# Optimization experiments

Measured on AMD Instinct MI355X. Metric: run time of the kernel, lower is better.

Reference implementation:

```python
import jax, jax.numpy as jnp
import numpy as np
from jax import lax

VOCAB, EMBED_DIM, NUM_TAGS = 50000, 300, 16
BATCH, SEQ = 64, 512


def setup_inputs() -> dict:
    key = jax.random.key(0)
    k0, k1, k2, k3, k4 = jax.random.split(key, 5)
    text = jax.random.randint(k0, (BATCH, SEQ), 0, VOCAB)
    tags = jax.random.randint(k1, (BATCH, SEQ), 0, NUM_TAGS)
    embed_table = jax.random.normal(k2, (VOCAB, EMBED_DIM), jnp.float32) * 0.02
    W = jax.random.normal(k3, (EMBED_DIM, NUM_TAGS), jnp.float32) * 0.05
    b = jnp.zeros((NUM_TAGS,), jnp.float32)
    trans = jax.random.uniform(k4, (NUM_TAGS, NUM_TAGS), jnp.float32)
    return {"text": text, "tags": tags, "embed_table": embed_table, "W": W, "b": b, "trans": trans}


def crf_log_likelihood(probs, tags, lens, trans):
    # probs: [B,S,T] unary potentials; tags: [B,S] int; lens: [B]; trans: [T,T]
    B, S, T = probs.shape
    t_idx = jnp.arange(S)
    mask = (t_idx[None, :] < lens[:, None])  # [B,S] valid positions

    # --- gold sequence score ---
    unary = jnp.take_along_axis(probs, tags[..., None], axis=2)[..., 0]  # [B,S]
    unary_score = jnp.sum(unary * mask, axis=1)
    btrans = trans[tags[:, :-1], tags[:, 1:]]            # [B,S-1]
    bmask = mask[:, 1:]                                   # transition t->t+1 valid iff t+1 < len
    binary_score = jnp.sum(btrans * bmask, axis=1)

    # --- forward algorithm (log partition) ---
    alpha0 = probs[:, 0]                                  # [B,T]
    emits = jnp.moveaxis(probs[:, 1:], 0, 1)              # [S-1,B,T]
    ms = jnp.moveaxis(mask[:, 1:], 0, 1)                  # [S-1,B]

    def step(alpha, inp):
        emit, m = inp
        new = jax.nn.logsumexp(alpha[:, :, None] + trans[None, :, :], axis=1) + emit
        return jnp.where(m[:, None], new, alpha), None

    alpha, _ = lax.scan(step, alpha0, (emits, ms))
    log_norm = jax.nn.logsumexp(alpha, axis=-1)           # [B]
    return unary_score + binary_score - log_norm


def reference(text, tags, embed_table, W, b, trans):
    # dropout is identity in eval/reference mode
    text_lens = jnp.sum((text != 0).astype(jnp.int32), axis=1)  # [B]
    probs = embed_table[text] @ W + b                            # [B,S,T]
    log_likelihood = crf_log_likelihood(probs, tags, text_lens, trans)
    return probs, text_lens, log_likelihood
```

## Files before the change

### kernel.cpp

```cpp
#include <hip/hip_runtime.h>
#include <hip/hip_bf16.h>

#define VOCAB 50000
#define ED    300
#define NT    16
#define BB    64
#define SS    512

#define LOG2E 1.4426950408889634f
#define LN2   0.6931471805599453f
#define WSTR  308

__global__ __launch_bounds__(256) void probs_kernel(const int* __restrict__ text,
                                                    const float* __restrict__ emb,
                                                    const float* __restrict__ W,
                                                    const float* __restrict__ bias,
                                                    float* __restrict__ out_probs) {
  __shared__ float wt[NT * WSTR];

  const int tid = threadIdx.x;
  const int lane = tid & 63, wave = tid >> 6;
  const int r = lane >> 4, t = lane & 15;
  const int row = blockIdx.x * 16 + wave * 4 + r;

  for (int e = tid; e < ED * NT; e += 256) {
    int d = e >> 4, tt = e & 15;
    wt[tt * WSTR + d] = W[e];
  }

  const int tok = text[row];
  const float4* erow = (const float4*)(emb + (size_t)tok * ED);
  float acc = bias[t];

  float4 A[8];
#pragma unroll
  for (int i = 0; i < 8; ++i) A[i] = erow[i];

  __syncthreads();

  const float4* w4 = (const float4*)(wt + t * WSTR);
#pragma unroll
  for (int c = 0; c < 75; ++c) {
    float4 e = A[c & 7];
    if (c < 67) A[c & 7] = erow[c + 8];
    float4 w = w4[c];
    acc = fmaf(e.x, w.x, acc);
    acc = fmaf(e.y, w.y, acc);
    acc = fmaf(e.z, w.z, acc);
    acc = fmaf(e.w, w.w, acc);
  }
  out_probs[(size_t)row * NT + t] = acc;
}

template <int CTRL>
__device__ __forceinline__ float dppmov(float x) {
  int xi = __float_as_int(x);
  return __int_as_float(
      __builtin_amdgcn_update_dpp(xi, xi, CTRL, 0xF, 0xF, false));
}

__device__ __forceinline__ float crf_step(float g, float pe, const float E[16]) {
  float gn, h, m, c, a1, a2, a3;
  asm("s_nop 1\n\t"
      "v_mov_b32_dpp %[h], %[g] row_half_mirror row_mask:0xf bank_mask:0xf\n\t"
      "v_mov_b32_dpp %[m], %[g] row_mirror row_mask:0xf bank_mask:0xf\n\t"
      "v_mul_f32 %[gn], %[g], %[e0]\n\t"
      "v_fmac_f32_dpp %[gn], %[g], %[e1] quad_perm:[1,0,3,2] row_mask:0xf bank_mask:0xf\n\t"
      "v_fmac_f32_dpp %[gn], %[g], %[e2] quad_perm:[2,3,0,1] row_mask:0xf bank_mask:0xf\n\t"
      "v_fmac_f32_dpp %[gn], %[g], %[e3] quad_perm:[3,2,1,0] row_mask:0xf bank_mask:0xf\n\t"
      "v_mov_b32_dpp %[c], %[m] row_half_mirror row_mask:0xf bank_mask:0xf\n\t"
      "v_mul_f32 %[a1], %[h], %[e7]\n\t"
      "v_fmac_f32_dpp %[a1], %[h], %[e6] quad_perm:[1,0,3,2] row_mask:0xf bank_mask:0xf\n\t"
      "v_fmac_f32_dpp %[a1], %[h], %[e5] quad_perm:[2,3,0,1] row_mask:0xf bank_mask:0xf\n\t"
      "v_fmac_f32_dpp %[a1], %[h], %[e4] quad_perm:[3,2,1,0] row_mask:0xf bank_mask:0xf\n\t"
      "v_mul_f32 %[a2], %[m], %[e15]\n\t"
      "v_fmac_f32_dpp %[a2], %[m], %[e14] quad_perm:[1,0,3,2] row_mask:0xf bank_mask:0xf\n\t"
      "v_fmac_f32_dpp %[a2], %[m], %[e13] quad_perm:[2,3,0,1] row_mask:0xf bank_mask:0xf\n\t"
      "v_fmac_f32_dpp %[a2], %[m], %[e12] quad_perm:[3,2,1,0] row_mask:0xf bank_mask:0xf\n\t"
      "v_mul_f32 %[a3], %[c], %[e8]\n\t"
      "v_fmac_f32_dpp %[a3], %[c], %[e9] quad_perm:[1,0,3,2] row_mask:0xf bank_mask:0xf\n\t"
      "v_fmac_f32_dpp %[a3], %[c], %[e10] quad_perm:[2,3,0,1] row_mask:0xf bank_mask:0xf\n\t"
      "v_fmac_f32_dpp %[a3], %[c], %[e11] quad_perm:[3,2,1,0] row_mask:0xf bank_mask:0xf\n\t"
      "v_add_f32 %[gn], %[gn], %[a1]\n\t"
      "v_add_f32 %[a2], %[a2], %[a3]\n\t"
      "v_add_f32 %[gn], %[gn], %[a2]\n\t"
      "v_mul_f32 %[gn], %[gn], %[pe]"
      : [gn] "=&v"(gn), [h] "=&v"(h), [m] "=&v"(m), [c] "=&v"(c),
        [a1] "=&v"(a1), [a2] "=&v"(a2), [a3] "=&v"(a3)
      : [g] "v"(g), [pe] "v"(pe),
        [e0] "v"(E[0]), [e1] "v"(E[1]), [e2] "v"(E[2]), [e3] "v"(E[3]),
        [e4] "v"(E[4]), [e5] "v"(E[5]), [e6] "v"(E[6]), [e7] "v"(E[7]),
        [e8] "v"(E[8]), [e9] "v"(E[9]), [e10] "v"(E[10]), [e11] "v"(E[11]),
        [e12] "v"(E[12]), [e13] "v"(E[13]), [e14] "v"(E[14]), [e15] "v"(E[15]));
  return gn;
}

__global__ __launch_bounds__(64) void crf_kernel(const int* __restrict__ text,
                                                 const int* __restrict__ tags,
                                                 const float* __restrict__ trans,
                                                 const float* __restrict__ probs,
                                                 float* __restrict__ out_lens,
                                                 float* __restrict__ out_ll) {
  const int tid = threadIdx.x;
  const int j = tid & 15;
  const int b = blockIdx.x;

  const int* tx = text + b * SS;
  int cz = 0;
#pragma unroll
  for (int k = 0; k < 8; ++k) cz += (tx[tid + 64 * k] != 0) ? 1 : 0;
  for (int off = 32; off > 0; off >>= 1) cz += __shfl_xor(cz, off, 64);
  const int len = cz;
  if (tid == 0) out_lens[b] = (float)len;

  const int* tg = tags + b * SS;
  int tgv[8];
  float sb = 0.f;
#pragma unroll
  for (int it = 0; it < 8; ++it) {
    const int s = tid + 64 * it;
    tgv[it] = tg[s];
    if (s >= 1 && s < len) sb += trans[tg[s - 1] * 16 + tgv[it]];
  }

  float E[16];
#pragma unroll
  for (int k = 0; k < 16; ++k) E[k] = __expf(trans[((j ^ k) << 4) + j]) * 0.03125f;

  const float* pb = probs + (size_t)b * SS * NT;

  float g = exp2f(pb[j] * LOG2E);
  float K2 = 0.f;

  const int T = (len > 0) ? len - 1 : 0;
  const int nfull = T >> 4;
  const int rem = T & 15;

  float raw[16];
#pragma unroll
  for (int c = 0; c < 16; ++c) raw[c] = pb[(1 + c) * NT + j] * LOG2E;

  int s0 = 1;
  for (int blk = 0; blk < nfull; ++blk) {
#pragma unroll
    for (int c = 0; c < 16; ++c) {
      float pe = exp2f(raw[c]);
      raw[c] = pb[(s0 + 16 + c) * NT + j] * LOG2E;
      g = crf_step(g, pe, E);
    }
    if ((blk & 3) == 3) {
      float mx = g;
      mx = fmaxf(mx, dppmov<0xB1>(mx));
      mx = fmaxf(mx, dppmov<0x4E>(mx));
      mx = fmaxf(mx, dppmov<0x141>(mx));
      mx = fmaxf(mx, dppmov<0x140>(mx));
      float rr = 1.0f / mx;
      K2 -= __log2f(rr);
      g *= rr;
    }
    s0 += 16;
  }
  for (int c = 0; c < rem; ++c) {
    float pe = exp2f(raw[c]);
    g = crf_step(g, pe, E);
  }

  float su = 0.f;
#pragma unroll
  for (int it = 0; it < 8; ++it) {
    const int s = tid + 64 * it;
    if (s < len) su += pb[s * NT + tgv[it]];
  }
  float sc = su + sb;
  for (int off = 32; off > 0; off >>= 1) sc += __shfl_xor(sc, off, 64);

  float x = g;
  x += dppmov<0xB1>(x);
  x += dppmov<0x4E>(x);
  x += dppmov<0x141>(x);
  x += dppmov<0x140>(x);
  float log_norm = LN2 * (K2 + 5.0f * (float)T + __log2f(x));
  if (tid == 0) out_ll[b] = sc - log_norm;
}

extern "C" void kernel_launch(void* const* d_in, const int* in_sizes, int n_in,
                              void* d_out, int out_size, void* d_ws, size_t ws_size,
                              hipStream_t stream) {
  const int* text = (const int*)d_in[0];
  const int* tags = (const int*)d_in[1];
  const float* emb = (const float*)d_in[2];
  const float* W = (const float*)d_in[3];
  const float* bias = (const float*)d_in[4];
  const float* trans = (const float*)d_in[5];

  float* out = (float*)d_out;
  float* out_probs = out;
  float* out_lens = out + BB * SS * NT;
  float* out_ll = out + BB * SS * NT + BB;

  probs_kernel<<<(BB * SS) / 16, 256, 0, stream>>>(text, emb, W, bias, out_probs);
  crf_kernel<<<BB, 64, 0, stream>>>(text, tags, trans, out_probs, out_lens, out_ll);
}
```

Before: 154.7 us.

## Parallelize CRF forward scan by chunking sequence into segment transfer matrices

Result: faster. 138.4 us (median of 2 runs) (-10.5%).

```diff
diff --git a/kernel.cpp b/kernel.cpp
--- a/kernel.cpp
+++ b/kernel.cpp
@@ -57,6 +57,14 @@
   int xi = __float_as_int(x);
   return __int_as_float(
       __builtin_amdgcn_update_dpp(xi, xi, CTRL, 0xF, 0xF, false));
+}
+
+__device__ __forceinline__ float max16(float x) {
+  x = fmaxf(x, dppmov<0xB1>(x));
+  x = fmaxf(x, dppmov<0x4E>(x));
+  x = fmaxf(x, dppmov<0x141>(x));
+  x = fmaxf(x, dppmov<0x140>(x));
+  return x;
 }
 
 __device__ __forceinline__ float crf_step(float g, float pe, const float E[16]) {
@@ -95,12 +103,98 @@
   return gn;
 }
 
-__global__ __launch_bounds__(64) void crf_kernel(const int* __restrict__ text,
-                                                 const int* __restrict__ tags,
-                                                 const float* __restrict__ trans,
-                                                 const float* __restrict__ probs,
-                                                 float* __restrict__ out_lens,
-                                                 float* __restrict__ out_ll) {
+__global__ __launch_bounds__(256) void seg_kernel(const int* __restrict__ text,
+                                                  const float* __restrict__ trans,
+                                                  const float* __restrict__ probs,
+                                                  float* __restrict__ gm,
+                                                  float* __restrict__ scl) {
+  __shared__ float pe_lds[128 * 16];
+  __shared__ float xsc[4][16 * 17];
+
+  const int tid = threadIdx.x;
+  const int lane = tid & 63;
+  const int w = tid >> 6;
+  const int q = lane >> 4;
+  const int j = lane & 15;
+  const int b = blockIdx.x >> 2;
+  const int q4 = blockIdx.x & 3;
+  const int seg = q4 * 4 + w;
+  const int s_start = 1 + 32 * seg;
+  const int segsz = (seg == 15) ? 31 : 32;
+
+  {
+    const float4* src = (const float4*)(probs + (size_t)b * SS * NT + (1 + 128 * q4) * NT);
+    float4* dst = (float4*)pe_lds;
+#pragma unroll
+    for (int i = 0; i < 2; ++i) {
+      float4 v = src[tid + 256 * i];
+      v.x = exp2f(v.x * LOG2E);
+      v.y = exp2f(v.y * LOG2E);
+      v.z = exp2f(v.z * LOG2E);
+      v.w = exp2f(v.w * LOG2E);
+      dst[tid + 256 * i] = v;
+    }
+  }
+
+  const int* tx = text + b * SS;
+  int cz = 0;
+#pragma unroll
+  for (int k = 0; k < 8; ++k) cz += (tx[lane + 64 * k] != 0) ? 1 : 0;
+  for (int off = 32; off > 0; off >>= 1) cz += __shfl_xor(cz, off, 64);
+  const int len = cz;
+
+  float E[16];
+#pragma unroll
+  for (int k = 0; k < 16; ++k) E[k] = __expf(trans[((j ^ k) << 4) + j]) * 0.03125f;
+
+  __syncthreads();
+
+  float g0 = (j == 4 * q + 0) ? 1.f : 0.f;
+  float g1 = (j == 4 * q + 1) ? 1.f : 0.f;
+  float g2 = (j == 4 * q + 2) ? 1.f : 0.f;
+  float g3 = (j == 4 * q + 3) ? 1.f : 0.f;
+
+  int na = len - s_start;
+  na = (na < 0) ? 0 : ((na > segsz) ? segsz : na);
+
+  const int row0 = 32 * w;
+  for (int it = 0; it < na; ++it) {
+    float pe = pe_lds[(row0 + it) * NT + j];
+    g0 = crf_step(g0, pe, E);
+    g1 = crf_step(g1, pe, E);
+    g2 = crf_step(g2, pe, E);
+    g3 = crf_step(g3, pe, E);
+  }
+
+  float mx = fmaxf(fmaxf(g0, g1), fmaxf(g2, g3));
+  mx = max16(mx);
+  mx = fmaxf(mx, __shfl_xor(mx, 16, 64));
+  mx = fmaxf(mx, __shfl_xor(mx, 32, 64));
+  float rr = 1.0f / mx;
+  g0 *= rr; g1 *= rr; g2 *= rr; g3 *= rr;
+
+  float* xs = xsc[w];
+  xs[(4 * q + 0) * 17 + j] = g0;
+  xs[(4 * q + 1) * 17 + j] = g1;
+  xs[(4 * q + 2) * 17 + j] = g2;
+  xs[(4 * q + 3) * 17 + j] = g3;
+  float* outm = gm + ((size_t)(b * 16 + seg)) * 256;
+#pragma unroll
+  for (int r = 0; r < 4; ++r) {
+    const int m = 4 * q + r;
+    outm[m * 16 + j] = xs[(j ^ m) * 17 + j];
+  }
+  if (lane == 0) scl[b * 16 + seg] = __log2f(mx);
+}
+
+__global__ __launch_bounds__(64) void crf2_kernel(const int* __restrict__ text,
+                                                  const int* __restrict__ tags,
+                                                  const float* __restrict__ trans,
+                                                  const float* __restrict__ probs,
+                                                  const float* __restrict__ gm,
+                                                  const float* __restrict__ scl,
+                                                  float* __restrict__ out_lens,
+                                                  float* __restrict__ out_ll) {
   const int tid = threadIdx.x;
   const int j = tid & 15;
   const int b = blockIdx.x;
@@ -123,46 +217,40 @@
     if (s >= 1 && s < len) sb += trans[tg[s - 1] * 16 + tgv[it]];
   }
 
-  float E[16];
-#pragma unroll
-  for (int k = 0; k < 16; ++k) E[k] = __expf(trans[((j ^ k) << 4) + j]) * 0.03125f;
-
   const float* pb = probs + (size_t)b * SS * NT;
+  const float* gb = gm + (size_t)b * 16 * 256;
+
+  float K2 = 0.f;
+#pragma unroll
+  for (int k = 0; k < 16; ++k) K2 += scl[b * 16 + k];
 
   float g = exp2f(pb[j] * LOG2E);
-  float K2 = 0.f;
-
-  const int T = (len > 0) ? len - 1 : 0;
-  const int nfull = T >> 4;
-  const int rem = T & 15;
-
-  float raw[16];
-#pragma unroll
-  for (int c = 0; c < 16; ++c) raw[c] = pb[(1 + c) * NT + j] * LOG2E;
-
-  int s0 = 1;
-  for (int blk = 0; blk < nfull; ++blk) {
-#pragma unroll
-    for (int c = 0; c < 16; ++c) {
-      float pe = exp2f(raw[c]);
-      raw[c] = pb[(s0 + 16 + c) * NT + j] * LOG2E;
-      g = crf_step(g, pe, E);
-    }
-    if ((blk & 3) == 3) {
-      float mx = g;
-      mx = fmaxf(mx, dppmov<0xB1>(mx));
-      mx = fmaxf(mx, dppmov<0x4E>(mx));
-      mx = fmaxf(mx, dppmov<0x141>(mx));
-      mx = fmaxf(mx, dppmov<0x140>(mx));
+
+  float EA[16], EB[16];
+#pragma unroll
+  for (int m = 0; m < 16; ++m) EA[m] = gb[m * 16 + j];
+
+  for (int k = 0; k < 16; k += 2) {
+#pragma unroll
+    for (int m = 0; m < 16; ++m) EB[m] = gb[(k + 1) * 256 + m * 16 + j];
+    g = crf_step(g, 1.0f, EA);
+    {
+      float mx = max16(g);
       float rr = 1.0f / mx;
       K2 -= __log2f(rr);
       g *= rr;
     }
-    s0 += 16;
-  }
-  for (int c = 0; c < rem; ++c) {
-    float pe = exp2f(raw[c]);
-    g = crf_step(g, pe, E);
+    if (k < 14) {
+#pragma unroll
+      for (int m = 0; m < 16; ++m) EA[m] = gb[(k + 2) * 256 + m * 16 + j];
+    }
+    g = crf_step(g, 1.0f, EB);
+    {
+      float mx = max16(g);
+      float rr = 1.0f / mx;
+      K2 -= __log2f(rr);
+      g *= rr;
+    }
   }
 
   float su = 0.f;
@@ -174,6 +262,7 @@
   float sc = su + sb;
   for (int off = 32; off > 0; off >>= 1) sc += __shfl_xor(sc, off, 64);
 
+  const int T = (len > 0) ? len - 1 : 0;
   float x = g;
   x += dppmov<0xB1>(x);
   x += dppmov<0x4E>(x);
@@ -198,6 +287,11 @@
   float* out_lens = out + BB * SS * NT;
   float* out_ll = out + BB * SS * NT + BB;
 
+  float* gm = (float*)d_ws;
+  float* scl = gm + BB * 16 * 256;
+
   probs_kernel<<<(BB * SS) / 16, 256, 0, stream>>>(text, emb, W, bias, out_probs);
-  crf_kernel<<<BB, 64, 0, stream>>>(text, tags, trans, out_probs, out_lens, out_ll);
-}
+  seg_kernel<<<BB * 4, 256, 0, stream>>>(text, trans, out_probs, gm, scl);
+  crf2_kernel<<<BB, 64, 0, stream>>>(text, tags, trans, out_probs, gm, scl,
+                                     out_lens, out_ll);
+}
```
